# Kernel tuning notes

Measured on AMD Instinct MI355X. Metric: run time of the kernel, lower is better.

Reference implementation:

```python
import jax, jax.numpy as jnp
import numpy as np

NEG_SLOPE = 0.01  # nn.LeakyReLU default


def _quantize_weight(w, bits):
    """Brevitas-style per-tensor symmetric narrow-range weight quantization.
    scale = max|w| / (2^(bits-1)-1); w_q = clip(round(w/scale)) * scale."""
    n = float(2 ** (bits - 1) - 1)
    scale = jnp.max(jnp.abs(w)) / n
    q = jnp.clip(jnp.round(w / scale), -n, n)
    return q * scale


def setup_inputs() -> dict:
    key = jax.random.key(0)
    ks = jax.random.split(key, 7)
    N, D_in, D_out = 32768, 1024, 2048
    x = jax.random.normal(ks[0], (N, D_in), dtype=jnp.float32)
    # He-ish init scaling for stability
    W0 = jax.random.normal(ks[1], (D_out, D_in), dtype=jnp.float32) * (1.0 / np.sqrt(D_in))
    b0 = jax.random.normal(ks[2], (D_out,), dtype=jnp.float32) * 0.01
    W1 = jax.random.normal(ks[3], (D_out, D_out), dtype=jnp.float32) * (1.0 / np.sqrt(D_out))
    b1 = jax.random.normal(ks[4], (D_out,), dtype=jnp.float32) * 0.01
    W2 = jax.random.normal(ks[5], (D_out, D_out), dtype=jnp.float32) * (1.0 / np.sqrt(D_out))
    b2 = jax.random.normal(ks[6], (D_out,), dtype=jnp.float32) * 0.01
    return {"x": x, "W0": W0, "b0": b0, "W1": W1, "b1": b1, "W2": W2, "b2": b2}


def reference(x, W0, b0, W1, b1, W2, b2):
    # Layer 0: QuantLinear with default 8-bit weights, then LeakyReLU, dropout(p=0)=id
    h = jnp.dot(x, _quantize_weight(W0, 8).T) + b0
    h = jnp.where(h >= 0, h, NEG_SLOPE * h)
    # Layers 1..2: 4-bit quantized weights
    for W, b in ((W1, b1), (W2, b2)):
        h = jnp.dot(h, _quantize_weight(W, 4).T) + b
        h = jnp.where(h >= 0, h, NEG_SLOPE * h)
    return h
```

## Files before the change

kernel.cpp:

```cpp
#include <hip/hip_runtime.h>
#include <hip/hip_bf16.h>
#include <stdint.h>

typedef __bf16 bf16x8 __attribute__((ext_vector_type(8)));
typedef float  f32x4  __attribute__((ext_vector_type(4)));
typedef unsigned short u16;

__device__ __forceinline__ u16 f2bf(float f) {
    return __builtin_bit_cast(u16, __float2bfloat16(f));
}

__device__ __forceinline__ void gload16(const void* g, void* l) {
    __builtin_amdgcn_global_load_lds(
        (const __attribute__((address_space(1))) void*)g,
        (__attribute__((address_space(3))) void*)l,
        16, 0, 0);
}


__global__ void zero3_k(unsigned int* p) {
    if (threadIdx.x < 3) p[threadIdx.x] = 0u;
}

__global__ void maxabs_k(const float* __restrict__ w, int n, unsigned int* __restrict__ out) {
    const int tid = threadIdx.x;
    float m = 0.f;
    for (int i = blockIdx.x * blockDim.x + tid; i < n; i += gridDim.x * blockDim.x)
        m = fmaxf(m, fabsf(w[i]));
    #pragma unroll
    for (int off = 32; off > 0; off >>= 1)
        m = fmaxf(m, __shfl_down(m, off));
    __shared__ float red[4];
    if ((tid & 63) == 0) red[tid >> 6] = m;
    __syncthreads();
    if (tid == 0) {
        m = fmaxf(fmaxf(red[0], red[1]), fmaxf(red[2], red[3]));
        atomicMax(out, __float_as_uint(m));
    }
}

__global__ void quant_k(const float* __restrict__ w, int n,
                        const unsigned int* __restrict__ maxbits, float qn,
                        u16* __restrict__ out) {
    const float scale = __uint_as_float(*maxbits) / qn;
    for (int i = blockIdx.x * blockDim.x + threadIdx.x; i < n; i += gridDim.x * blockDim.x) {
        float q = rintf(w[i] / scale);
        q = fminf(qn, fmaxf(-qn, q));
        out[i] = f2bf(q * scale);
    }
}

__global__ void cvt_k(const float* __restrict__ x, u16* __restrict__ o, long n) {
    const long stride = (long)gridDim.x * blockDim.x * 4;
    for (long i = ((long)blockIdx.x * blockDim.x + threadIdx.x) * 4; i < n; i += stride) {
        float4 v = *(const float4*)(x + i);
        unsigned int lo = (unsigned int)f2bf(v.x) | ((unsigned int)f2bf(v.y) << 16);
        unsigned int hi = (unsigned int)f2bf(v.z) | ((unsigned int)f2bf(v.w) << 16);
        *(uint2*)(o + i) = make_uint2(lo, hi);
    }
}


#define BARR  __builtin_amdgcn_s_barrier()
#define VM4   asm volatile("s_waitcnt vmcnt(4)" ::: "memory")
#define LGKM0 do { asm volatile("s_waitcnt lgkmcnt(0)" ::: "memory");          \
                   __builtin_amdgcn_sched_barrier(0); } while (0)
#define FENCE asm volatile("" ::: "memory")

#define STG(kt, ISA, h)                                                        \
  do {                                                                         \
    const u16* _s = (ISA) ? gA : gB;                                           \
    u16* _d = smem + ((ISA) ? 0 : 32768) + (((kt) & 1) << 14) + ((h) << 13)    \
              + wave * 512;                                                    \
    const size_t _go = (size_t)((h) * 128) * K + (size_t)(kt) * 64;            \
    gload16(_s + _go,                 _d);                                     \
    gload16(_s + _go + (size_t)64 * K, _d + 4096);                             \
  } while (0)

#define RD_A(kt, mh)                                                           \
  do {                                                                         \
    const u16* _p = smem + (((kt) & 1) << 14) + ((mh) << 13) + rowA;           \
    _Pragma("unroll") for (int m2 = 0; m2 < 4; ++m2) {                         \
        afr[m2 * 2]     = *(const bf16x8*)(_p + m2 * 2048 + g0);               \
        afr[m2 * 2 + 1] = *(const bf16x8*)(_p + m2 * 2048 + g1);               \
    }                                                                          \
  } while (0)

#define RD_B(kt, nh, DST)                                                      \
  do {                                                                         \
    const u16* _p = smem + 32768 + (((kt) & 1) << 14) + ((nh) << 13) + rowB;   \
    _Pragma("unroll") for (int n2 = 0; n2 < 2; ++n2) {                         \
        DST[n2 * 2]     = *(const bf16x8*)(_p + n2 * 4096 + g0);               \
        DST[n2 * 2 + 1] = *(const bf16x8*)(_p + n2 * 4096 + g1);               \
    }                                                                          \
  } while (0)

#define MM(mh, nh, BS)                                                         \
  do {                                                                         \
    __builtin_amdgcn_s_setprio(1);                                             \
    _Pragma("unroll") for (int m2 = 0; m2 < 4; ++m2)                           \
      _Pragma("unroll") for (int n2 = 0; n2 < 2; ++n2) {                       \
        acc[(mh)*4+m2][(nh)*2+n2] = __builtin_amdgcn_mfma_f32_16x16x32_bf16(   \
            afr[m2*2],     BS[n2*2],   acc[(mh)*4+m2][(nh)*2+n2], 0, 0, 0);    \
        acc[(mh)*4+m2][(nh)*2+n2] = __builtin_amdgcn_mfma_f32_16x16x32_bf16(   \
            afr[m2*2+1],   BS[n2*2+1], acc[(mh)*4+m2][(nh)*2+n2], 0, 0, 0);    \
      }                                                                        \
    __builtin_amdgcn_s_setprio(0);                                             \
  } while (0)

template<int BF16OUT>
__global__ __launch_bounds__(512, 2)
void gemm8x(const u16* __restrict__ A, const u16* __restrict__ B,
            const float* __restrict__ bias, void* __restrict__ Cv,
            int M, int Nn, int K)
{
    __shared__ __align__(128) u16 smem[65536];

    const int tid  = threadIdx.x;
    const int lane = tid & 63;
    const int wave = tid >> 6;
    const int wm = wave >> 2;
    const int wn = wave & 3;

    const int nbx = Nn >> 8;
    const int cpx = gridDim.x >> 3;
    const int swz = (blockIdx.x & 7) * cpx + (blockIdx.x >> 3);
    const int bn = (swz % nbx) << 8;
    const int bm = (swz / nbx) << 8;

    const int scol = (((tid & 7) ^ ((tid >> 4) & 7)) << 3);
    const u16* gA = A + (size_t)(bm + (tid >> 3)) * K + scol;
    const u16* gB = B + (size_t)(bn + (tid >> 3)) * K + scol;

    const int fr = lane & 15;
    const int g0 = (((lane >> 4)    ) ^ (fr >> 1)) << 3;
    const int g1 = (((lane >> 4) + 4) ^ (fr >> 1)) << 3;
    const int rowA = (wm * 16 + fr) << 6;
    const int rowB = (wn * 16 + fr) << 6;

    f32x4 acc[8][4] = {};
    bf16x8 afr[8], b0f[4], b1f[4];

    const int NT = K >> 6;

    STG(0, 1, 0); STG(0, 0, 0); STG(0, 0, 1); STG(0, 1, 1);
    VM4;
    BARR;

    for (int kt = 0; kt < NT - 1; ++kt) {
        RD_A(kt, 0); RD_B(kt, 0, b0f);
        STG(kt + 1, 1, 0);
        VM4; BARR; LGKM0;
        MM(0, 0, b0f);
        FENCE;
        RD_B(kt, 1, b1f);
        STG(kt + 1, 0, 0);
        VM4; BARR; LGKM0;
        MM(0, 1, b1f);
        FENCE;
        RD_A(kt, 1);
        STG(kt + 1, 0, 1);
        BARR; LGKM0;
        MM(1, 0, b0f);
        FENCE;
        STG(kt + 1, 1, 1);
        VM4; BARR;
        __builtin_amdgcn_sched_barrier(0);
        MM(1, 1, b1f);
        FENCE;
    }
    {
        const int kt = NT - 1;
        RD_A(kt, 0); RD_B(kt, 0, b0f);
        asm volatile("s_waitcnt vmcnt(2)" ::: "memory");
        BARR; LGKM0;
        MM(0, 0, b0f);
        FENCE;
        RD_B(kt, 1, b1f);
        asm volatile("s_waitcnt vmcnt(0)" ::: "memory");
        BARR; LGKM0;
        MM(0, 1, b1f);
        FENCE;
        RD_A(kt, 1);
        BARR; LGKM0;
        MM(1, 0, b0f);
        FENCE;
        __builtin_amdgcn_sched_barrier(0);
        MM(1, 1, b1f);
    }

    const int crow = (lane >> 4) << 2;
    const int ccol = lane & 15;
    #pragma unroll
    for (int n = 0; n < 4; ++n) {
        const int col = bn + n * 64 + wn * 16 + ccol;
        const float bv = bias[col];
        #pragma unroll
        for (int m = 0; m < 8; ++m) {
            const int row0 = bm + (m >> 2) * 128 + (m & 3) * 32 + wm * 16 + crow;
            #pragma unroll
            for (int j = 0; j < 4; ++j) {
                float v = acc[m][n][j] + bv;
                v = (v >= 0.f) ? v : 0.01f * v;
                if (BF16OUT) {
                    ((u16*)Cv)[(size_t)(row0 + j) * Nn + col] = f2bf(v);
                } else {
                    ((float*)Cv)[(size_t)(row0 + j) * Nn + col] = v;
                }
            }
        }
    }
}


extern "C" void kernel_launch(void* const* d_in, const int* in_sizes, int n_in,
                              void* d_out, int out_size, void* d_ws, size_t ws_size,
                              hipStream_t stream) {
    const float* x  = (const float*)d_in[0];
    const float* W0 = (const float*)d_in[1];
    const float* b0 = (const float*)d_in[2];
    const float* W1 = (const float*)d_in[3];
    const float* b1 = (const float*)d_in[4];
    const float* W2 = (const float*)d_in[5];
    const float* b2 = (const float*)d_in[6];

    const int N = 32768, D0 = 1024, D1 = 2048;

    char* ws = (char*)d_ws;
    u16* xbf = (u16*)ws;  ws += (size_t)N * D0 * 2;
    u16* h0  = (u16*)ws;  ws += (size_t)N * D1 * 2;
    u16* h1  = (u16*)ws;  ws += (size_t)N * D1 * 2;
    u16* w0q = (u16*)ws;  ws += (size_t)D1 * D0 * 2;
    u16* w1q = (u16*)ws;  ws += (size_t)D1 * D1 * 2;
    u16* w2q = (u16*)ws;  ws += (size_t)D1 * D1 * 2;
    unsigned int* scales = (unsigned int*)ws;

    zero3_k<<<1, 64, 0, stream>>>(scales);
    maxabs_k<<<256, 256, 0, stream>>>(W0, D1 * D0, scales + 0);
    maxabs_k<<<256, 256, 0, stream>>>(W1, D1 * D1, scales + 1);
    maxabs_k<<<256, 256, 0, stream>>>(W2, D1 * D1, scales + 2);
    quant_k<<<2048, 256, 0, stream>>>(W0, D1 * D0, scales + 0, 127.f, w0q);
    quant_k<<<2048, 256, 0, stream>>>(W1, D1 * D1, scales + 1, 7.f, w1q);
    quant_k<<<2048, 256, 0, stream>>>(W2, D1 * D1, scales + 2, 7.f, w2q);
    cvt_k<<<4096, 256, 0, stream>>>(x, xbf, (long)N * D0);

    const int blocks = (D1 / 256) * (N / 256);
    gemm8x<1><<<blocks, 512, 0, stream>>>(xbf, w0q, b0, h0, N, D1, D0);
    gemm8x<1><<<blocks, 512, 0, stream>>>(h0, w1q, b1, h1, N, D1, D1);
    gemm8x<0><<<blocks, 512, 0, stream>>>(h1, w2q, b2, d_out, N, D1, D1);
}
```

Baseline: 723.0 us.

## Double-buffer A fragments and overlap LDS reads with MFMA in GEMM loop

Splits the A register fragment into two buffers so the second A half can be read from LDS while MFMAs on the first half run. It reorders each k-step so LDS reads are issued before the preceding MFMA block, and drops the sched_barrier in the wait macro and one block barrier. The aim is to hide LDS latency behind matrix math. In exchange it uses more VGPRs, which risks spills under the 512x2 launch bounds, and the changed barrier placement could leave hazards on the LDS double buffer.

```diff
diff --git a/kernel.cpp b/kernel.cpp
--- a/kernel.cpp
+++ b/kernel.cpp
@@ -62,9 +62,8 @@
 
 
 #define BARR  __builtin_amdgcn_s_barrier()
-#define VM4   asm volatile("s_waitcnt vmcnt(4)" ::: "memory")
-#define LGKM0 do { asm volatile("s_waitcnt lgkmcnt(0)" ::: "memory");          \
-                   __builtin_amdgcn_sched_barrier(0); } while (0)
+#define VMW(N) asm volatile("s_waitcnt vmcnt(" #N ")" ::: "memory")
+#define LGKM0 asm volatile("s_waitcnt lgkmcnt(0)" ::: "memory")
 #define FENCE asm volatile("" ::: "memory")
 
 #define STG(kt, ISA, h)                                                        \
@@ -77,12 +76,12 @@
     gload16(_s + _go + (size_t)64 * K, _d + 4096);                             \
   } while (0)
 
-#define RD_A(kt, mh)                                                           \
+#define RD_A(kt, mh, DST)                                                      \
   do {                                                                         \
     const u16* _p = smem + (((kt) & 1) << 14) + ((mh) << 13) + rowA;           \
     _Pragma("unroll") for (int m2 = 0; m2 < 4; ++m2) {                         \
-        afr[m2 * 2]     = *(const bf16x8*)(_p + m2 * 2048 + g0);               \
-        afr[m2 * 2 + 1] = *(const bf16x8*)(_p + m2 * 2048 + g1);               \
+        DST[m2 * 2]     = *(const bf16x8*)(_p + m2 * 2048 + g0);               \
+        DST[m2 * 2 + 1] = *(const bf16x8*)(_p + m2 * 2048 + g1);               \
     }                                                                          \
   } while (0)
 
@@ -95,15 +94,15 @@
     }                                                                          \
   } while (0)
 
-#define MM(mh, nh, BS)                                                         \
+#define MM(mh, nh, AS, BS)                                                     \
   do {                                                                         \
     __builtin_amdgcn_s_setprio(1);                                             \
     _Pragma("unroll") for (int m2 = 0; m2 < 4; ++m2)                           \
       _Pragma("unroll") for (int n2 = 0; n2 < 2; ++n2) {                       \
         acc[(mh)*4+m2][(nh)*2+n2] = __builtin_amdgcn_mfma_f32_16x16x32_bf16(   \
-            afr[m2*2],     BS[n2*2],   acc[(mh)*4+m2][(nh)*2+n2], 0, 0, 0);    \
+            AS[m2*2],     BS[n2*2],   acc[(mh)*4+m2][(nh)*2+n2], 0, 0, 0);     \
         acc[(mh)*4+m2][(nh)*2+n2] = __builtin_amdgcn_mfma_f32_16x16x32_bf16(   \
-            afr[m2*2+1],   BS[n2*2+1], acc[(mh)*4+m2][(nh)*2+n2], 0, 0, 0);    \
+            AS[m2*2+1],   BS[n2*2+1], acc[(mh)*4+m2][(nh)*2+n2], 0, 0, 0);     \
       }                                                                        \
     __builtin_amdgcn_s_setprio(0);                                             \
   } while (0)
@@ -139,54 +138,51 @@
     const int rowB = (wn * 16 + fr) << 6;
 
     f32x4 acc[8][4] = {};
-    bf16x8 afr[8], b0f[4], b1f[4];
+    bf16x8 aA[8], aB[8], b0f[4], b1f[4];
 
     const int NT = K >> 6;
 
     STG(0, 1, 0); STG(0, 0, 0); STG(0, 0, 1); STG(0, 1, 1);
-    VM4;
-    BARR;
+    VMW(4);
+    BARR; FENCE;
 
     for (int kt = 0; kt < NT - 1; ++kt) {
-        RD_A(kt, 0); RD_B(kt, 0, b0f);
+        RD_A(kt, 0, aA); RD_B(kt, 0, b0f);
         STG(kt + 1, 1, 0);
-        VM4; BARR; LGKM0;
-        MM(0, 0, b0f);
-        FENCE;
+        VMW(4);
+        LGKM0;
+        BARR; FENCE;
         RD_B(kt, 1, b1f);
+        MM(0, 0, aA, b0f);
         STG(kt + 1, 0, 0);
-        VM4; BARR; LGKM0;
-        MM(0, 1, b1f);
-        FENCE;
-        RD_A(kt, 1);
+        VMW(4);
+        LGKM0;
+        BARR; FENCE;
+        RD_A(kt, 1, aB);
+        MM(0, 1, aA, b1f);
         STG(kt + 1, 0, 1);
-        BARR; LGKM0;
-        MM(1, 0, b0f);
-        FENCE;
+        MM(1, 0, aB, b0f);
         STG(kt + 1, 1, 1);
-        VM4; BARR;
-        __builtin_amdgcn_sched_barrier(0);
-        MM(1, 1, b1f);
-        FENCE;
+        VMW(4);
+        LGKM0;
+        BARR; FENCE;
+        MM(1, 1, aB, b1f);
     }
     {
         const int kt = NT - 1;
-        RD_A(kt, 0); RD_B(kt, 0, b0f);
-        asm volatile("s_waitcnt vmcnt(2)" ::: "memory");
-        BARR; LGKM0;
-        MM(0, 0, b0f);
-        FENCE;
+        RD_A(kt, 0, aA); RD_B(kt, 0, b0f);
+        VMW(2);
+        LGKM0;
+        BARR; FENCE;
         RD_B(kt, 1, b1f);
-        asm volatile("s_waitcnt vmcnt(0)" ::: "memory");
-        BARR; LGKM0;
-        MM(0, 1, b1f);
-        FENCE;
-        RD_A(kt, 1);
-        BARR; LGKM0;
-        MM(1, 0, b0f);
-        FENCE;
-        __builtin_amdgcn_sched_barrier(0);
-        MM(1, 1, b1f);
+        MM(0, 0, aA, b0f);
+        VMW(0);
+        LGKM0;
+        BARR; FENCE;
+        RD_A(kt, 1, aB);
+        MM(0, 1, aA, b1f);
+        MM(1, 0, aB, b0f);
+        MM(1, 1, aB, b1f);
     }
 
     const int crow = (lane >> 4) << 2;
```

Result: no change. 732.4 us (+1.3%).
